# Kernel optimization log

Measured on AMD Instinct MI355X. Metric: run time of the kernel, lower is better.

## Reference

```python
import jax, jax.numpy as jnp
import numpy as np

ALPHA = 0.2      # LeakyReLU negative slope
BN_EPS = 1e-5    # torch BatchNorm1d default eps

N_NODES = 50000
N_EDGES = 1600000
DIM_IN = 128
DIM_HID = 64
DIM_OUT = 128
NUM_HEADS = 8


def gat_layer(feat, src, dst, W, a, gamma, beta):
    """One GATLayer forward (dropout disabled, BatchNorm in training mode
    i.e. normalized with batch statistics over the node dimension)."""
    n = feat.shape[0]
    dh = W.shape[1]
    msg = feat @ W                                  # [N, dh]
    attn_src = msg @ a[:dh]                         # [N]
    attn_dst = msg @ a[dh:]                         # [N]
    scores = jax.nn.leaky_relu(attn_src[src] + attn_dst[dst], ALPHA)  # [E]
    scores = scores - scores.max()                  # global max-subtract (as in source)
    e = jnp.exp(scores)                             # [E]
    denom = jax.ops.segment_sum(e, dst, num_segments=n) + 1e-10       # [N]
    coef = e / denom[dst]                           # [E] segment-softmax
    out = jax.ops.segment_sum(msg[src] * coef[:, None], dst, num_segments=n)  # [N, dh]
    # BatchNorm1d (training-mode batch stats, biased variance)
    mean = out.mean(axis=0)
    var = out.var(axis=0)
    out = (out - mean) * jax.lax.rsqrt(var + BN_EPS) * gamma + beta
    return out


def setup_inputs() -> dict:
    key = jax.random.key(0)
    ks = jax.random.split(key, 10)
    feat = jax.random.normal(ks[0], (N_NODES, DIM_IN), dtype=jnp.float32)
    edges = jax.random.randint(ks[1], (2, N_EDGES), 0, N_NODES)

    def xavier(k, shape):
        fan_in, fan_out = shape[0], shape[-1]
        lim = np.sqrt(6.0 / (fan_in + fan_out)).astype(np.float32)
        return jax.random.uniform(k, shape, jnp.float32, -lim, lim)

    W_heads = xavier(ks[2], (NUM_HEADS, DIM_IN, DIM_HID))
    a_heads = xavier(ks[3], (NUM_HEADS, 2 * DIM_HID))
    gamma_h = jnp.ones((NUM_HEADS, DIM_HID), jnp.float32)
    beta_h = jnp.zeros((NUM_HEADS, DIM_HID), jnp.float32)
    W_out = xavier(ks[4], (NUM_HEADS * DIM_HID, DIM_OUT))
    a_out = xavier(ks[5], (2 * DIM_OUT,))
    gamma_o = jnp.ones((DIM_OUT,), jnp.float32)
    beta_o = jnp.zeros((DIM_OUT,), jnp.float32)
    W_res = xavier(ks[6], (DIM_IN, DIM_OUT))
    b_res = jnp.zeros((DIM_OUT,), jnp.float32)
    return {"feat": feat, "edges": edges, "W_heads": W_heads, "a_heads": a_heads,
            "gamma_h": gamma_h, "beta_h": beta_h, "W_out": W_out, "a_out": a_out,
            "gamma_o": gamma_o, "beta_o": beta_o, "W_res": W_res, "b_res": b_res}


def reference(feat, edges, W_heads, a_heads, gamma_h, beta_h,
              W_out, a_out, gamma_o, beta_o, W_res, b_res):
    src, dst = edges[0], edges[1]
    # python loop over a small fixed number of heads keeps peak memory low
    head_outs = [gat_layer(feat, src, dst, W_heads[h], a_heads[h], gamma_h[h], beta_h[h])
                 for h in range(NUM_HEADS)]
    x = jnp.concatenate(head_outs, axis=-1)          # [N, H*dh]
    x = gat_layer(x, src, dst, W_out, a_out, gamma_o, beta_o)  # [N, dout]
    x = x + feat @ W_res + b_res                     # residual Linear
    return x
```

## Files before the change

### kernel.cpp

```cpp
#include <hip/hip_runtime.h>
#include <math.h>

#define N_NODES 50000
#define N_EDGES 1600000
#define DIM_IN  128
#define DIM_HID 64
#define NHEADS  8
#define HDIM    (NHEADS*DIM_HID)
#define DIM_OUT 128
#define SMBLK   1024
#define MAXBLK  512
#define HISTBLK 2048
#define LDK     72
#define INV_N   2e-5f
#define CSBLK   400

typedef __attribute__((ext_vector_type(2))) unsigned short us2;
typedef __attribute__((ext_vector_type(4))) unsigned short us4;
typedef __attribute__((ext_vector_type(8))) unsigned short us8;
typedef __attribute__((ext_vector_type(8))) short bf16x8;
typedef __attribute__((ext_vector_type(4))) float f32x4;

__device__ __forceinline__ float leaky(float x) { return x >= 0.f ? x : 0.2f * x; }
__device__ __forceinline__ float bf2f(unsigned short h) {
  return __uint_as_float(((unsigned)h) << 16);
}
__device__ __forceinline__ unsigned short f2bf(float f) {
  unsigned u = __float_as_uint(f);
  unsigned r = (u + 0x7fffu + ((u >> 16) & 1u)) >> 16;
  return (unsigned short)r;
}
__device__ __forceinline__ float bn_scale(float sum, float sq, float g) {
  float mean = sum * INV_N;
  float var = sq * INV_N - mean * mean;
  return g * rsqrtf(var + 1e-5f);
}

__global__ void prep_kernel(const float* __restrict__ feat, const float* __restrict__ Wh,
                            const float* __restrict__ Wres, const int* __restrict__ edst,
                            unsigned short* __restrict__ feat_bf,
                            unsigned short* __restrict__ Bt1,
                            unsigned short* __restrict__ Btr,
                            int* __restrict__ counts) {
  int b = blockIdx.x;
  if (b < 6250) {
    int i = b * 256 + threadIdx.x;
    float4 v = *reinterpret_cast<const float4*>(&feat[(size_t)i * 4]);
    us4 o;
    o[0] = f2bf(v.x); o[1] = f2bf(v.y); o[2] = f2bf(v.z); o[3] = f2bf(v.w);
    *reinterpret_cast<us4*>(&feat_bf[(size_t)i * 4]) = o;
  } else if (b < 6506) {
    int idx = (b - 6250) * 256 + threadIdx.x;
    int n = idx >> 7, k = idx & 127;
    Bt1[idx] = f2bf(Wh[(n >> 6) * (DIM_IN * DIM_HID) + k * DIM_HID + (n & 63)]);
  } else if (b < 6570) {
    int idx = (b - 6506) * 256 + threadIdx.x;
    int n = idx >> 7, k = idx & 127;
    Btr[idx] = f2bf(Wres[k * DIM_OUT + n]);
  } else {
    int bid = b - 6570;
    for (int e = bid * 256 + threadIdx.x; e < N_EDGES; e += HISTBLK * 256)
      atomicAdd(&counts[edst[e]], 1);
  }
}

__global__ void foldw2_kernel(const float* __restrict__ W,
                              const float* __restrict__ colsum, const float* __restrict__ colsq,
                              const float* __restrict__ gamma,
                              unsigned short* __restrict__ Bt) {
  int idx = blockIdx.x * 256 + threadIdx.x;
  if (idx >= DIM_OUT * HDIM) return;
  int n = idx >> 9, k = idx & 511;
  float sc = bn_scale(colsum[k], colsq[k], gamma[k]);
  Bt[idx] = f2bf(W[k * DIM_OUT + n] * sc);
}

__global__ void bias2_kernel(const float* __restrict__ W,
                             const float* __restrict__ colsum, const float* __restrict__ colsq,
                             const float* __restrict__ gamma, const float* __restrict__ beta,
                             float* __restrict__ bias2) {
  int j = threadIdx.x;
  if (j >= DIM_OUT) return;
  float s = 0.f;
  for (int c = 0; c < HDIM; ++c) {
    float mean = colsum[c] * INV_N;
    float sc = bn_scale(colsum[c], colsq[c], gamma[c]);
    float shift = beta[c] - mean * sc;
    s = fmaf(shift, W[c * DIM_OUT + j], s);
  }
  bias2[j] = s;
}

__device__ __forceinline__ void gemm_body(
    const unsigned short* __restrict__ A, const unsigned short* __restrict__ Bt,
    void* __restrict__ Cout, const float* __restrict__ bias,
    int M, int N, int K, int outbf) {
  __shared__ unsigned short As[128 * LDK];
  __shared__ unsigned short Bs[128 * LDK];
  const int tid = threadIdx.x;
  const int lane = tid & 63, wid = tid >> 6;
  const int wr = wid >> 1, wc = wid & 1;
  const int l15 = lane & 15, lhi = lane >> 4;
  const int m0 = blockIdx.y * 128, n0 = blockIdx.x * 128;
  const int srow = tid >> 3;
  const int sc8 = (tid - srow) & 7;
  f32x4 acc[4][4];
#pragma unroll
  for (int i = 0; i < 4; ++i)
#pragma unroll
    for (int j = 0; j < 4; ++j) acc[i][j] = f32x4{0.f, 0.f, 0.f, 0.f};

  for (int k0 = 0; k0 < K; k0 += 64) {
    __syncthreads();
#pragma unroll
    for (int p = 0; p < 4; ++p) {
      int row = p * 32 + srow;
      us8 va = {0, 0, 0, 0, 0, 0, 0, 0};
      int gr = m0 + row;
      if (gr < M) va = *reinterpret_cast<const us8*>(&A[(size_t)gr * K + k0 + sc8 * 8]);
      *reinterpret_cast<us8*>(&As[row * LDK + sc8 * 8]) = va;
      us8 vb = {0, 0, 0, 0, 0, 0, 0, 0};
      int gn = n0 + row;
      if (gn < N) vb = *reinterpret_cast<const us8*>(&Bt[(size_t)gn * K + k0 + sc8 * 8]);
      *reinterpret_cast<us8*>(&Bs[row * LDK + sc8 * 8]) = vb;
    }
    __syncthreads();
#pragma unroll
    for (int kk = 0; kk < 2; ++kk) {
      bf16x8 af[4], bfr[4];
#pragma unroll
      for (int i = 0; i < 4; ++i)
        af[i] = *reinterpret_cast<const bf16x8*>(&As[(wr * 64 + i * 16 + l15) * LDK + kk * 32 + lhi * 8]);
#pragma unroll
      for (int j = 0; j < 4; ++j)
        bfr[j] = *reinterpret_cast<const bf16x8*>(&Bs[(wc * 64 + j * 16 + l15) * LDK + kk * 32 + lhi * 8]);
#pragma unroll
      for (int i = 0; i < 4; ++i)
#pragma unroll
        for (int j = 0; j < 4; ++j)
          acc[i][j] = __builtin_amdgcn_mfma_f32_16x16x32_bf16(af[i], bfr[j], acc[i][j], 0, 0, 0);
    }
  }
#pragma unroll
  for (int j = 0; j < 4; ++j) {
    int col = n0 + wc * 64 + j * 16 + l15;
    float bb = bias ? bias[col] : 0.f;
#pragma unroll
    for (int i = 0; i < 4; ++i) {
      f32x4 v = acc[i][j];
#pragma unroll
      for (int t = 0; t < 4; ++t) {
        int row = m0 + wr * 64 + i * 16 + lhi * 4 + t;
        if (row < M) {
          float o = v[t] + bb;
          if (outbf) ((unsigned short*)Cout)[(size_t)row * N + col] = f2bf(o);
          else       ((float*)Cout)[(size_t)row * N + col] = o;
        }
      }
    }
  }
}

__global__ __launch_bounds__(256) void gemm_single(
    const unsigned short* __restrict__ A, const unsigned short* __restrict__ Bt,
    void* __restrict__ Cout, const float* __restrict__ bias,
    int M, int N, int K, int outbf) {
  gemm_body(A, Bt, Cout, bias, M, N, K, outbf);
}

__global__ __launch_bounds__(256) void gemm_dual(
    const unsigned short* __restrict__ A0, const unsigned short* __restrict__ Bt0,
    void* __restrict__ C0, const float* __restrict__ b0, int K0,
    const unsigned short* __restrict__ A1, const unsigned short* __restrict__ Bt1,
    void* __restrict__ C1, const float* __restrict__ b1, int K1) {
  if (blockIdx.z == 0) gemm_body(A0, Bt0, C0, b0, N_NODES, DIM_OUT, K0, 1);
  else                 gemm_body(A1, Bt1, C1, b1, N_NODES, DIM_OUT, K1, 0);
}

__global__ __launch_bounds__(256) void attn1_kernel(
    const unsigned short* __restrict__ msg, const float* __restrict__ a_heads,
    float* __restrict__ asrc, float* __restrict__ adst, int Nn) {
  int lane = threadIdx.x & 63;
  int n = blockIdx.x * 4 + (threadIdx.x >> 6);
  if (n >= Nn) return;
  us8 v = *reinterpret_cast<const us8*>(&msg[(size_t)n * HDIM + lane * 8]);
  int h = lane >> 3, p0 = (lane & 7) * 8;
  float s = 0.f, d = 0.f;
#pragma unroll
  for (int j = 0; j < 8; ++j) {
    float f = bf2f(v[j]);
    s = fmaf(f, a_heads[h * 128 + p0 + j], s);
    d = fmaf(f, a_heads[h * 128 + 64 + p0 + j], d);
  }
  s += __shfl_xor(s, 1, 64); s += __shfl_xor(s, 2, 64); s += __shfl_xor(s, 4, 64);
  d += __shfl_xor(d, 1, 64); d += __shfl_xor(d, 2, 64); d += __shfl_xor(d, 4, 64);
  if ((lane & 7) == 0) { asrc[n * 8 + h] = s; adst[n * 8 + h] = d; }
}

__global__ __launch_bounds__(256) void attn2_kernel(
    const unsigned short* __restrict__ msg, const float* __restrict__ a_out,
    float* __restrict__ asrc, float* __restrict__ adst, int Nn) {
  int lane = threadIdx.x & 63;
  int n = blockIdx.x * 4 + (threadIdx.x >> 6);
  if (n >= Nn) return;
  us2 v = *reinterpret_cast<const us2*>(&msg[(size_t)n * 128 + lane * 2]);
  float f0 = bf2f(v[0]), f1 = bf2f(v[1]);
  float s = f0 * a_out[2 * lane] + f1 * a_out[2 * lane + 1];
  float d = f0 * a_out[128 + 2 * lane] + f1 * a_out[128 + 2 * lane + 1];
#pragma unroll
  for (int off = 32; off; off >>= 1) {
    s += __shfl_xor(s, off, 64);
    d += __shfl_xor(d, off, 64);
  }
  if (lane == 0) { asrc[n] = s; adst[n] = d; }
}

__global__ __launch_bounds__(256) void scan1_kernel(
    const int* __restrict__ counts, int* __restrict__ rowptr, int* __restrict__ bsum, int n) {
  __shared__ int wsum[4];
  int b0 = blockIdx.x * 1024;
  int t = threadIdx.x;
  int lane = t & 63, w = t >> 6;
  int v[4]; int s = 0;
#pragma unroll
  for (int i = 0; i < 4; ++i) {
    int idx = b0 + t * 4 + i;
    v[i] = (idx < n) ? counts[idx] : 0;
    s += v[i];
  }
  int x = s;
#pragma unroll
  for (int off = 1; off < 64; off <<= 1) {
    int y = __shfl_up(x, off, 64);
    if (lane >= off) x += y;
  }
  if (lane == 63) wsum[w] = x;
  __syncthreads();
  int wof = 0;
  for (int i = 0; i < w; ++i) wof += wsum[i];
  int run = wof + x - s;
#pragma unroll
  for (int i = 0; i < 4; ++i) {
    int idx = b0 + t * 4 + i;
    if (idx < n) rowptr[idx] = run;
    run += v[i];
  }
  if (t == 255) bsum[blockIdx.x] = wof + x;
}

__global__ __launch_bounds__(256) void scan23_kernel(
    int* __restrict__ rowptr, const int* __restrict__ bsum, int n) {
  __shared__ int carry_sh;
  int b = blockIdx.x, t = threadIdx.x;
  if (t < 64) {
    int v = (t < b) ? bsum[t] : 0;
#pragma unroll
    for (int off = 32; off; off >>= 1) v += __shfl_xor(v, off, 64);
    if (t == 0) carry_sh = v;
  }
  __syncthreads();
  int carry = carry_sh;
  int i0 = b * 1024;
#pragma unroll
  for (int q = 0; q < 4; ++q) {
    int i = i0 + q * 256 + t;
    if (i < n) rowptr[i] += carry;
  }
  if (b == gridDim.x - 1 && t == 0) rowptr[n] = N_EDGES;
}

__global__ __launch_bounds__(256) void scatter_max1_kernel(
    const int* __restrict__ esrc, const int* __restrict__ edst,
    const float* __restrict__ asrc, const float* __restrict__ adst,
    const int* __restrict__ rowptr, int* __restrict__ cursor,
    int* __restrict__ colsrc, float* __restrict__ part, int E) {
  float m[8];
#pragma unroll
  for (int h = 0; h < 8; ++h) m[h] = -3.4e38f;
  for (int e = blockIdx.x * blockDim.x + threadIdx.x; e < E; e += gridDim.x * blockDim.x) {
    int s = esrc[e], d = edst[e];
    int pos = rowptr[d] + atomicAdd(&cursor[d], 1);
    colsrc[pos] = s;
    float4 s0 = *reinterpret_cast<const float4*>(&asrc[(size_t)s * 8]);
    float4 s1 = *reinterpret_cast<const float4*>(&asrc[(size_t)s * 8 + 4]);
    float4 d0 = *reinterpret_cast<const float4*>(&adst[(size_t)d * 8]);
    float4 d1 = *reinterpret_cast<const float4*>(&adst[(size_t)d * 8 + 4]);
    float xs[8] = {s0.x + d0.x, s0.y + d0.y, s0.z + d0.z, s0.w + d0.w,
                   s1.x + d1.x, s1.y + d1.y, s1.z + d1.z, s1.w + d1.w};
#pragma unroll
    for (int h = 0; h < 8; ++h) m[h] = fmaxf(m[h], leaky(xs[h]));
  }
#pragma unroll
  for (int h = 0; h < 8; ++h)
#pragma unroll
    for (int off = 32; off; off >>= 1) m[h] = fmaxf(m[h], __shfl_xor(m[h], off, 64));
  __shared__ float sm[4][8];
  int wv = threadIdx.x >> 6, ln = threadIdx.x & 63;
  if (ln == 0)
#pragma unroll
    for (int h = 0; h < 8; ++h) sm[wv][h] = m[h];
  __syncthreads();
  if (threadIdx.x < 8) {
    int h = threadIdx.x;
    part[blockIdx.x * 8 + h] =
        fmaxf(fmaxf(sm[0][h], sm[1][h]), fmaxf(sm[2][h], sm[3][h]));
  }
}

__global__ void max1_final_kernel(const float* __restrict__ part, float* __restrict__ maxv, int nblk) {
  int t = threadIdx.x;
  int h = t & 7, k = t >> 3;
  float m = -3.4e38f;
  for (int i = k; i < nblk; i += 8) m = fmaxf(m, part[i * 8 + h]);
  m = fmaxf(m, __shfl_xor(m, 8, 64));
  m = fmaxf(m, __shfl_xor(m, 16, 64));
  m = fmaxf(m, __shfl_xor(m, 32, 64));
  if (t < 8) maxv[t] = m;
}

__global__ __launch_bounds__(256) void max2_part_kernel(
    const int* __restrict__ esrc, const int* __restrict__ edst,
    const float* __restrict__ asrc, const float* __restrict__ adst,
    float* __restrict__ part, int E) {
  float m = -3.4e38f;
  for (int e = blockIdx.x * blockDim.x + threadIdx.x; e < E; e += gridDim.x * blockDim.x) {
    float x = asrc[esrc[e]] + adst[edst[e]];
    m = fmaxf(m, leaky(x));
  }
#pragma unroll
  for (int off = 32; off; off >>= 1) m = fmaxf(m, __shfl_xor(m, off, 64));
  __shared__ float sm[4];
  int wv = threadIdx.x >> 6, ln = threadIdx.x & 63;
  if (ln == 0) sm[wv] = m;
  __syncthreads();
  if (threadIdx.x == 0)
    part[blockIdx.x] = fmaxf(fmaxf(sm[0], sm[1]), fmaxf(sm[2], sm[3]));
}

__global__ void max2_final_kernel(const float* __restrict__ part, float* __restrict__ maxv, int nblk) {
  int t = threadIdx.x;
  float m = -3.4e38f;
  for (int i = t; i < nblk; i += 64) m = fmaxf(m, part[i]);
#pragma unroll
  for (int off = 32; off; off >>= 1) m = fmaxf(m, __shfl_xor(m, off, 64));
  if (t == 0) maxv[0] = m;
}

__global__ __launch_bounds__(256) void agg1_kernel(
    const unsigned short* __restrict__ msg, const float* __restrict__ asrc,
    const float* __restrict__ adst, const float* __restrict__ maxv,
    const int* __restrict__ rowptr, const int* __restrict__ colsrc,
    unsigned short* __restrict__ out) {
  int wv = threadIdx.x >> 6, l = threadIdx.x & 63;
  int n = blockIdx.x * 4 + wv;
  const int h = l >> 3;
  const int eloc = l & 7;
  const int hbase = l & 56;
  float M = maxv[h];
  float ad = adst[(size_t)n * 8 + h];
  int e0 = rowptr[n], e1 = rowptr[n + 1];
  float acc[8];
#pragma unroll
  for (int j = 0; j < 8; ++j) acc[j] = 0.f;
  float ds = 0.f;
  int base = e0;
  for (; base + 8 <= e1; base += 8) {
    int sreg = colsrc[base + eloc];
    float x = asrc[(size_t)sreg * 8 + h] + ad;
    x = x >= 0.f ? x : 0.2f * x;
    float creg = __expf(x - M);
#pragma unroll
    for (int e = 0; e < 8; ++e) {
      float c = __shfl(creg, hbase | e, 64);
      int s = __shfl(sreg, e, 64);
      ds += c;
      us8 m = *reinterpret_cast<const us8*>(&msg[(size_t)s * HDIM + l * 8]);
#pragma unroll
      for (int j = 0; j < 8; ++j) acc[j] = fmaf(bf2f(m[j]), c, acc[j]);
    }
  }
  if (base < e1) {
    int cnt = e1 - base;
    int sreg = 0; float creg = 0.f;
    if (eloc < cnt) {
      sreg = colsrc[base + eloc];
      float x = asrc[(size_t)sreg * 8 + h] + ad;
      x = x >= 0.f ? x : 0.2f * x;
      creg = __expf(x - M);
    }
    for (int e = 0; e < cnt; ++e) {
      float c = __shfl(creg, hbase | e, 64);
      int s = __shfl(sreg, e, 64);
      ds += c;
      us8 m = *reinterpret_cast<const us8*>(&msg[(size_t)s * HDIM + l * 8]);
#pragma unroll
      for (int j = 0; j < 8; ++j) acc[j] = fmaf(bf2f(m[j]), c, acc[j]);
    }
  }
  float inv = 1.0f / (ds + 1e-10f);
  us8 o;
#pragma unroll
  for (int j = 0; j < 8; ++j) o[j] = f2bf(acc[j] * inv);
  *reinterpret_cast<us8*>(&out[(size_t)n * HDIM + l * 8]) = o;
}

__global__ __launch_bounds__(256) void agg2_kernel(
    const unsigned short* __restrict__ msg, const float* __restrict__ asrc,
    const float* __restrict__ adst, const float* __restrict__ maxv,
    const int* __restrict__ rowptr, const int* __restrict__ colsrc,
    float* __restrict__ out) {
  int wv = threadIdx.x >> 6, ln = threadIdx.x & 63;
  int n = blockIdx.x * 4 + wv;
  float M = maxv[0];
  float ad = adst[n];
  int e0 = rowptr[n], e1 = rowptr[n + 1];
  float a0 = 0.f, a1 = 0.f, ds = 0.f;
  for (int base = e0; base < e1; base += 64) {
    int cnt = min(64, e1 - base);
    int s_reg = 0; float c_reg = 0.f;
    if (ln < cnt) {
      s_reg = colsrc[base + ln];
      float x = asrc[s_reg] + ad;
      x = x >= 0.f ? x : 0.2f * x;
      c_reg = __expf(x - M);
    }
    int e = 0;
    for (; e + 4 <= cnt; e += 4) {
      int s0 = __shfl(s_reg, e, 64),     s1 = __shfl(s_reg, e + 1, 64);
      int s2 = __shfl(s_reg, e + 2, 64), s3 = __shfl(s_reg, e + 3, 64);
      float c0 = __shfl(c_reg, e, 64),     c1 = __shfl(c_reg, e + 1, 64);
      float c2 = __shfl(c_reg, e + 2, 64), c3 = __shfl(c_reg, e + 3, 64);
      us2 m0 = *reinterpret_cast<const us2*>(&msg[(size_t)s0 * 128 + 2 * ln]);
      us2 m1 = *reinterpret_cast<const us2*>(&msg[(size_t)s1 * 128 + 2 * ln]);
      us2 m2 = *reinterpret_cast<const us2*>(&msg[(size_t)s2 * 128 + 2 * ln]);
      us2 m3 = *reinterpret_cast<const us2*>(&msg[(size_t)s3 * 128 + 2 * ln]);
      ds += (c0 + c1) + (c2 + c3);
      a0 = fmaf(bf2f(m0[0]), c0, a0); a1 = fmaf(bf2f(m0[1]), c0, a1);
      a0 = fmaf(bf2f(m1[0]), c1, a0); a1 = fmaf(bf2f(m1[1]), c1, a1);
      a0 = fmaf(bf2f(m2[0]), c2, a0); a1 = fmaf(bf2f(m2[1]), c2, a1);
      a0 = fmaf(bf2f(m3[0]), c3, a0); a1 = fmaf(bf2f(m3[1]), c3, a1);
    }
    for (; e < cnt; ++e) {
      int s = __shfl(s_reg, e, 64);
      float c = __shfl(c_reg, e, 64);
      us2 m = *reinterpret_cast<const us2*>(&msg[(size_t)s * 128 + 2 * ln]);
      ds += c;
      a0 = fmaf(bf2f(m[0]), c, a0);
      a1 = fmaf(bf2f(m[1]), c, a1);
    }
  }
  float inv = 1.0f / (ds + 1e-10f);
  float2 r; r.x = a0 * inv; r.y = a1 * inv;
  *reinterpret_cast<float2*>(&out[(size_t)n * 128 + 2 * ln]) = r;
}

__global__ __launch_bounds__(256) void colstats_bf512_kernel(
    const unsigned short* __restrict__ X, float* __restrict__ sums,
    float* __restrict__ sqs, int M) {
  int tid = threadIdx.x;
  int cg = tid & 63;
  int wv = tid >> 6;
  int rows = (M + gridDim.x - 1) / gridDim.x;
  int r0 = blockIdx.x * rows;
  int r1 = min(M, r0 + rows);
  float s[8], q[8];
#pragma unroll
  for (int j = 0; j < 8; ++j) { s[j] = 0.f; q[j] = 0.f; }
  for (int r = r0 + wv; r < r1; r += 4) {
    us8 v = *reinterpret_cast<const us8*>(&X[(size_t)r * 512 + cg * 8]);
#pragma unroll
    for (int j = 0; j < 8; ++j) {
      float f = bf2f(v[j]);
      s[j] += f; q[j] = fmaf(f, f, q[j]);
    }
  }
  __shared__ float shs[3][512];
  __shared__ float shq[3][512];
  if (wv > 0) {
#pragma unroll
    for (int j = 0; j < 8; ++j) {
      shs[wv - 1][cg * 8 + j] = s[j];
      shq[wv - 1][cg * 8 + j] = q[j];
    }
  }
  __syncthreads();
  if (wv == 0) {
#pragma unroll
    for (int j = 0; j < 8; ++j) {
      int c = cg * 8 + j;
      atomicAdd(&sums[c], s[j] + shs[0][c] + shs[1][c] + shs[2][c]);
      atomicAdd(&sqs[c],  q[j] + shq[0][c] + shq[1][c] + shq[2][c]);
    }
  }
}

__global__ __launch_bounds__(256) void colstats_f128_kernel(
    const float* __restrict__ X, float* __restrict__ sums,
    float* __restrict__ sqs, int M) {
  int tid = threadIdx.x;
  int g = tid & 31;
  int slot = tid >> 5;
  int rows = (M + gridDim.x - 1) / gridDim.x;
  int r0 = blockIdx.x * rows;
  int r1 = min(M, r0 + rows);
  float s[4] = {0.f, 0.f, 0.f, 0.f}, q[4] = {0.f, 0.f, 0.f, 0.f};
  for (int r = r0 + slot; r < r1; r += 8) {
    float4 v = *reinterpret_cast<const float4*>(&X[(size_t)r * 128 + g * 4]);
    s[0] += v.x; q[0] = fmaf(v.x, v.x, q[0]);
    s[1] += v.y; q[1] = fmaf(v.y, v.y, q[1]);
    s[2] += v.z; q[2] = fmaf(v.z, v.z, q[2]);
    s[3] += v.w; q[3] = fmaf(v.w, v.w, q[3]);
  }
#pragma unroll
  for (int j = 0; j < 4; ++j) {
    s[j] += __shfl_xor(s[j], 32, 64);
    q[j] += __shfl_xor(q[j], 32, 64);
  }
  __shared__ float shs[3][128];
  __shared__ float shq[3][128];
  int wv = tid >> 6, ln = tid & 63;
  if (wv > 0 && ln < 32) {
#pragma unroll
    for (int j = 0; j < 4; ++j) {
      shs[wv - 1][g * 4 + j] = s[j];
      shq[wv - 1][g * 4 + j] = q[j];
    }
  }
  __syncthreads();
  if (wv == 0 && ln < 32) {
#pragma unroll
    for (int j = 0; j < 4; ++j) {
      int c = g * 4 + j;
      atomicAdd(&sums[c], s[j] + shs[0][c] + shs[1][c] + shs[2][c]);
      atomicAdd(&sqs[c],  q[j] + shq[0][c] + shq[1][c] + shq[2][c]);
    }
  }
}

__global__ void final_kernel(float* __restrict__ out, const float* __restrict__ resid,
                             const float* __restrict__ colsum, const float* __restrict__ colsq,
                             const float* __restrict__ gamma, const float* __restrict__ beta,
                             int total) {
  for (int i = blockIdx.x * blockDim.x + threadIdx.x; i < total; i += gridDim.x * blockDim.x) {
    int c = i & 127;
    float mean = colsum[c] * INV_N;
    float sc = bn_scale(colsum[c], colsq[c], gamma[c]);
    float sh = beta[c] - mean * sc;
    out[i] = fmaf(out[i], sc, sh) + resid[i];
  }
}

extern "C" void kernel_launch(void* const* d_in, const int* in_sizes, int n_in,
                              void* d_out, int out_size, void* d_ws, size_t ws_size,
                              hipStream_t stream) {
  const float* feat    = (const float*)d_in[0];
  const int*   edges   = (const int*)d_in[1];
  const int*   esrc    = edges;
  const int*   edst    = edges + N_EDGES;
  const float* W_heads = (const float*)d_in[2];
  const float* a_heads = (const float*)d_in[3];
  const float* gamma_h = (const float*)d_in[4];
  const float* beta_h  = (const float*)d_in[5];
  const float* W_out   = (const float*)d_in[6];
  const float* a_out   = (const float*)d_in[7];
  const float* gamma_o = (const float*)d_in[8];
  const float* beta_o  = (const float*)d_in[9];
  const float* W_res   = (const float*)d_in[10];
  const float* b_res   = (const float*)d_in[11];
  float* out = (float*)d_out;

  char* ws = (char*)d_ws;
  size_t off = 0;
  auto alloc = [&](size_t bytes) {
    void* p = ws + off;
    off = (off + bytes + 255) & ~(size_t)255;
    return p;
  };
  unsigned short* msg1    = (unsigned short*)alloc((size_t)N_NODES * HDIM * 2);
  unsigned short* out1_bf = (unsigned short*)alloc((size_t)N_NODES * HDIM * 2);
  unsigned short* feat_bf = (unsigned short*)alloc((size_t)N_NODES * DIM_IN * 2);
  float*    resid  = (float*)alloc((size_t)N_NODES * DIM_OUT * 4);
  float*    asrc1  = (float*)alloc((size_t)N_NODES * NHEADS * 4);
  float*    adst1  = (float*)alloc((size_t)N_NODES * NHEADS * 4);
  int*      counts = (int*)alloc((size_t)N_NODES * 4);
  int*      cursor = (int*)alloc((size_t)N_NODES * 4);
  int*      rowptr = (int*)alloc((size_t)(N_NODES + 1) * 4);
  int*      colsrc = (int*)alloc((size_t)N_EDGES * 4);
  int*      bsum   = (int*)alloc(64 * 4);
  float*    part   = (float*)alloc((size_t)SMBLK * 8 * 4);
  float*    maxv1  = (float*)alloc(8 * 4);
  float*    maxv2  = (float*)alloc(4);
  float*    colsum = (float*)alloc(HDIM * 4);
  float*    colsq  = (float*)alloc(HDIM * 4);
  unsigned short* Bt1 = (unsigned short*)alloc((size_t)HDIM * DIM_IN * 2);
  unsigned short* Bt2 = (unsigned short*)alloc((size_t)DIM_OUT * HDIM * 2);
  unsigned short* Btr = (unsigned short*)alloc((size_t)DIM_OUT * DIM_IN * 2);
  float*    bias2  = (float*)alloc(DIM_OUT * 4);
  unsigned short* msg2 = msg1;
  float* asrc2 = asrc1; float* adst2 = adst1;
  (void)n_in; (void)in_sizes; (void)out_size; (void)ws_size;

  hipMemsetAsync(counts, 0, (char*)rowptr - (char*)counts, stream);
  hipMemsetAsync(colsum, 0, 4096, stream);

  prep_kernel<<<6570 + HISTBLK, 256, 0, stream>>>(feat, W_heads, W_res, edst,
                                                  feat_bf, Bt1, Btr, counts);

  dim3 g1(HDIM / 128, (N_NODES + 127) / 128);
  gemm_single<<<g1, 256, 0, stream>>>(feat_bf, Bt1, msg1, nullptr, N_NODES, HDIM, DIM_IN, 1);
  attn1_kernel<<<(N_NODES + 3) / 4, 256, 0, stream>>>(msg1, a_heads, asrc1, adst1, N_NODES);

  int nsb = (N_NODES + 1023) / 1024;
  scan1_kernel<<<nsb, 256, 0, stream>>>(counts, rowptr, bsum, N_NODES);
  scan23_kernel<<<nsb, 256, 0, stream>>>(rowptr, bsum, N_NODES);

  scatter_max1_kernel<<<SMBLK, 256, 0, stream>>>(esrc, edst, asrc1, adst1, rowptr,
                                                 cursor, colsrc, part, N_EDGES);
  max1_final_kernel<<<1, 64, 0, stream>>>(part, maxv1, SMBLK);
  agg1_kernel<<<N_NODES / 4, 256, 0, stream>>>(msg1, asrc1, adst1, maxv1, rowptr, colsrc, out1_bf);

  colstats_bf512_kernel<<<CSBLK, 256, 0, stream>>>(out1_bf, colsum, colsq, N_NODES);
  foldw2_kernel<<<(DIM_OUT * HDIM + 255) / 256, 256, 0, stream>>>(W_out, colsum, colsq, gamma_h, Bt2);
  bias2_kernel<<<1, 128, 0, stream>>>(W_out, colsum, colsq, gamma_h, beta_h, bias2);

  dim3 g2d(1, (N_NODES + 127) / 128, 2);
  gemm_dual<<<g2d, 256, 0, stream>>>(out1_bf, Bt2, msg2, bias2, HDIM,
                                     feat_bf, Btr, resid, b_res, DIM_IN);
  attn2_kernel<<<(N_NODES + 3) / 4, 256, 0, stream>>>(msg2, a_out, asrc2, adst2, N_NODES);

  max2_part_kernel<<<MAXBLK, 256, 0, stream>>>(esrc, edst, asrc2, adst2, part, N_EDGES);
  max2_final_kernel<<<1, 64, 0, stream>>>(part, maxv2, MAXBLK);
  agg2_kernel<<<N_NODES / 4, 256, 0, stream>>>(msg2, asrc2, adst2, maxv2, rowptr, colsrc, out);

  hipMemsetAsync(colsum, 0, 4096, stream);
  colstats_f128_kernel<<<CSBLK, 256, 0, stream>>>(out, colsum, colsq, N_NODES);
  final_kernel<<<2048, 256, 0, stream>>>(out, resid, colsum, colsq, gamma_o, beta_o,
                                         N_NODES * DIM_OUT);
}
```

Measured before the change: 780.9 us.

## Fuse attention dots into GEMM epilogue and use node-level softmax shift

The per-head attention source/destination dot products are now computed in the first GEMM's epilogue from the accumulators, so the separate pass that re-reads the bf16 message matrix goes away. The global softmax shift no longer needs an edge-level gather. It is taken as max(asrc)+max(adst) from cheap node-level reductions, which relies on softmax being invariant to any constant shift. The edge scatter kernel no longer gathers attention values, and the second-layer edge max pass is gone. The trade-off is that the shift is only an approximate bound rather than the exact max (leaky is not applied), which slightly changes exp magnitudes and the relative size of the 1e-10 epsilon.

```diff
diff --git a/kernel.cpp b/kernel.cpp
--- a/kernel.cpp
+++ b/kernel.cpp
@@ -8,9 +8,9 @@
 #define NHEADS  8
 #define HDIM    (NHEADS*DIM_HID)
 #define DIM_OUT 128
-#define SMBLK   1024
-#define MAXBLK  512
+#define SCBLK   1024
 #define HISTBLK 2048
+#define NMBLK   64
 #define LDK     72
 #define INV_N   2e-5f
 #define CSBLK   400
@@ -161,11 +161,99 @@
   }
 }
 
-__global__ __launch_bounds__(256) void gemm_single(
+__global__ __launch_bounds__(256) void gemm1_attn_kernel(
     const unsigned short* __restrict__ A, const unsigned short* __restrict__ Bt,
-    void* __restrict__ Cout, const float* __restrict__ bias,
-    int M, int N, int K, int outbf) {
-  gemm_body(A, Bt, Cout, bias, M, N, K, outbf);
+    unsigned short* __restrict__ Cout, const float* __restrict__ a_heads,
+    float* __restrict__ asrc, float* __restrict__ adst) {
+  __shared__ unsigned short As[128 * LDK];
+  __shared__ unsigned short Bs[128 * LDK];
+  const int M = N_NODES, N = HDIM, K = DIM_IN;
+  const int tid = threadIdx.x;
+  const int lane = tid & 63, wid = tid >> 6;
+  const int wr = wid >> 1, wc = wid & 1;
+  const int l15 = lane & 15, lhi = lane >> 4;
+  const int m0 = blockIdx.y * 128, n0 = blockIdx.x * 128;
+  const int srow = tid >> 3;
+  const int sc8 = (tid - srow) & 7;
+  f32x4 acc[4][4];
+#pragma unroll
+  for (int i = 0; i < 4; ++i)
+#pragma unroll
+    for (int j = 0; j < 4; ++j) acc[i][j] = f32x4{0.f, 0.f, 0.f, 0.f};
+
+  for (int k0 = 0; k0 < K; k0 += 64) {
+    __syncthreads();
+#pragma unroll
+    for (int p = 0; p < 4; ++p) {
+      int row = p * 32 + srow;
+      us8 va = {0, 0, 0, 0, 0, 0, 0, 0};
+      int gr = m0 + row;
+      if (gr < M) va = *reinterpret_cast<const us8*>(&A[(size_t)gr * K + k0 + sc8 * 8]);
+      *reinterpret_cast<us8*>(&As[row * LDK + sc8 * 8]) = va;
+      us8 vb = {0, 0, 0, 0, 0, 0, 0, 0};
+      int gn = n0 + row;
+      if (gn < N) vb = *reinterpret_cast<const us8*>(&Bt[(size_t)gn * K + k0 + sc8 * 8]);
+      *reinterpret_cast<us8*>(&Bs[row * LDK + sc8 * 8]) = vb;
+    }
+    __syncthreads();
+#pragma unroll
+    for (int kk = 0; kk < 2; ++kk) {
+      bf16x8 af[4], bfr[4];
+#pragma unroll
+      for (int i = 0; i < 4; ++i)
+        af[i] = *reinterpret_cast<const bf16x8*>(&As[(wr * 64 + i * 16 + l15) * LDK + kk * 32 + lhi * 8]);
+#pragma unroll
+      for (int j = 0; j < 4; ++j)
+        bfr[j] = *reinterpret_cast<const bf16x8*>(&Bs[(wc * 64 + j * 16 + l15) * LDK + kk * 32 + lhi * 8]);
+#pragma unroll
+      for (int i = 0; i < 4; ++i)
+#pragma unroll
+        for (int j = 0; j < 4; ++j)
+          acc[i][j] = __builtin_amdgcn_mfma_f32_16x16x32_bf16(af[i], bfr[j], acc[i][j], 0, 0, 0);
+    }
+  }
+#pragma unroll
+  for (int j = 0; j < 4; ++j) {
+    int col = n0 + wc * 64 + j * 16 + l15;
+#pragma unroll
+    for (int i = 0; i < 4; ++i) {
+      f32x4 v = acc[i][j];
+#pragma unroll
+      for (int t = 0; t < 4; ++t) {
+        int row = m0 + wr * 64 + i * 16 + lhi * 4 + t;
+        if (row < M) Cout[(size_t)row * N + col] = f2bf(v[t]);
+      }
+    }
+  }
+  const int h = blockIdx.x * 2 + wc;
+  float aS[4], aD[4];
+#pragma unroll
+  for (int j = 0; j < 4; ++j) {
+    aS[j] = a_heads[h * 128 + j * 16 + l15];
+    aD[j] = a_heads[h * 128 + 64 + j * 16 + l15];
+  }
+#pragma unroll
+  for (int i = 0; i < 4; ++i) {
+#pragma unroll
+    for (int t = 0; t < 4; ++t) {
+      float s = 0.f, d = 0.f;
+#pragma unroll
+      for (int j = 0; j < 4; ++j) {
+        float v = acc[i][j][t];
+        s = fmaf(v, aS[j], s);
+        d = fmaf(v, aD[j], d);
+      }
+      s += __shfl_xor(s, 1, 64); s += __shfl_xor(s, 2, 64);
+      s += __shfl_xor(s, 4, 64); s += __shfl_xor(s, 8, 64);
+      d += __shfl_xor(d, 1, 64); d += __shfl_xor(d, 2, 64);
+      d += __shfl_xor(d, 4, 64); d += __shfl_xor(d, 8, 64);
+      int row = m0 + wr * 64 + i * 16 + lhi * 4 + t;
+      if (l15 == 0 && row < M) {
+        asrc[(size_t)row * 8 + h] = s;
+        adst[(size_t)row * 8 + h] = d;
+      }
+    }
+  }
 }
 
 __global__ __launch_bounds__(256) void gemm_dual(
@@ -175,26 +263,6 @@
     void* __restrict__ C1, const float* __restrict__ b1, int K1) {
   if (blockIdx.z == 0) gemm_body(A0, Bt0, C0, b0, N_NODES, DIM_OUT, K0, 1);
   else                 gemm_body(A1, Bt1, C1, b1, N_NODES, DIM_OUT, K1, 0);
-}
-
-__global__ __launch_bounds__(256) void attn1_kernel(
-    const unsigned short* __restrict__ msg, const float* __restrict__ a_heads,
-    float* __restrict__ asrc, float* __restrict__ adst, int Nn) {
-  int lane = threadIdx.x & 63;
-  int n = blockIdx.x * 4 + (threadIdx.x >> 6);
-  if (n >= Nn) return;
-  us8 v = *reinterpret_cast<const us8*>(&msg[(size_t)n * HDIM + lane * 8]);
-  int h = lane >> 3, p0 = (lane & 7) * 8;
-  float s = 0.f, d = 0.f;
-#pragma unroll
-  for (int j = 0; j < 8; ++j) {
-    float f = bf2f(v[j]);
-    s = fmaf(f, a_heads[h * 128 + p0 + j], s);
-    d = fmaf(f, a_heads[h * 128 + 64 + p0 + j], d);
-  }
-  s += __shfl_xor(s, 1, 64); s += __shfl_xor(s, 2, 64); s += __shfl_xor(s, 4, 64);
-  d += __shfl_xor(d, 1, 64); d += __shfl_xor(d, 2, 64); d += __shfl_xor(d, 4, 64);
-  if ((lane & 7) == 0) { asrc[n * 8 + h] = s; adst[n * 8 + h] = d; }
 }
 
 __global__ __launch_bounds__(256) void attn2_kernel(
@@ -215,6 +283,54 @@
   if (lane == 0) { asrc[n] = s; adst[n] = d; }
 }
 
+__global__ __launch_bounds__(256) void nodemax_part_kernel(
+    const float* __restrict__ a, const float* __restrict__ b,
+    float* __restrict__ part, int total) {
+  int t = threadIdx.x;
+  float ms = -3.4e38f, md = -3.4e38f;
+  for (int i = blockIdx.x * 256 + t; i < total; i += NMBLK * 256) {
+    ms = fmaxf(ms, a[i]);
+    md = fmaxf(md, b[i]);
+  }
+  ms = fmaxf(ms, __shfl_xor(ms, 8, 64));
+  ms = fmaxf(ms, __shfl_xor(ms, 16, 64));
+  ms = fmaxf(ms, __shfl_xor(ms, 32, 64));
+  md = fmaxf(md, __shfl_xor(md, 8, 64));
+  md = fmaxf(md, __shfl_xor(md, 16, 64));
+  md = fmaxf(md, __shfl_xor(md, 32, 64));
+  __shared__ float sh[4][8][2];
+  int wv = t >> 6, ln = t & 63;
+  if (ln < 8) { sh[wv][ln][0] = ms; sh[wv][ln][1] = md; }
+  __syncthreads();
+  if (t < 8) {
+    float s4 = fmaxf(fmaxf(sh[0][t][0], sh[1][t][0]), fmaxf(sh[2][t][0], sh[3][t][0]));
+    float d4 = fmaxf(fmaxf(sh[0][t][1], sh[1][t][1]), fmaxf(sh[2][t][1], sh[3][t][1]));
+    part[blockIdx.x * 16 + t * 2] = s4;
+    part[blockIdx.x * 16 + t * 2 + 1] = d4;
+  }
+}
+
+__global__ void nodemax_final_kernel(const float* __restrict__ part, float* __restrict__ maxv, int H) {
+  int t = threadIdx.x;
+  int ch = t & 15, k = t >> 4;
+  float m = -3.4e38f;
+  for (int i = k; i < NMBLK; i += 4) m = fmaxf(m, part[i * 16 + ch]);
+  m = fmaxf(m, __shfl_xor(m, 16, 64));
+  m = fmaxf(m, __shfl_xor(m, 32, 64));
+  float S = __shfl(m, (t & 7) * 2, 64);
+  float D = __shfl(m, (t & 7) * 2 + 1, 64);
+  if (H == 8) {
+    if (t < 8) maxv[t] = S + D;
+  } else {
+    float Sm = S, Dm = D;
+    Sm = fmaxf(Sm, __shfl_xor(Sm, 1, 64)); Sm = fmaxf(Sm, __shfl_xor(Sm, 2, 64));
+    Sm = fmaxf(Sm, __shfl_xor(Sm, 4, 64));
+    Dm = fmaxf(Dm, __shfl_xor(Dm, 1, 64)); Dm = fmaxf(Dm, __shfl_xor(Dm, 2, 64));
+    Dm = fmaxf(Dm, __shfl_xor(Dm, 4, 64));
+    if (t == 0) maxv[0] = Sm + Dm;
+  }
+}
+
 __global__ __launch_bounds__(256) void scan1_kernel(
     const int* __restrict__ counts, int* __restrict__ rowptr, int* __restrict__ bsum, int n) {
   __shared__ int wsum[4];
@@ -269,81 +385,15 @@
   if (b == gridDim.x - 1 && t == 0) rowptr[n] = N_EDGES;
 }
 
-__global__ __launch_bounds__(256) void scatter_max1_kernel(
+__global__ __launch_bounds__(256) void scatter_kernel(
     const int* __restrict__ esrc, const int* __restrict__ edst,
-    const float* __restrict__ asrc, const float* __restrict__ adst,
     const int* __restrict__ rowptr, int* __restrict__ cursor,
-    int* __restrict__ colsrc, float* __restrict__ part, int E) {
-  float m[8];
-#pragma unroll
-  for (int h = 0; h < 8; ++h) m[h] = -3.4e38f;
+    int* __restrict__ colsrc, int E) {
   for (int e = blockIdx.x * blockDim.x + threadIdx.x; e < E; e += gridDim.x * blockDim.x) {
-    int s = esrc[e], d = edst[e];
+    int d = edst[e];
     int pos = rowptr[d] + atomicAdd(&cursor[d], 1);
-    colsrc[pos] = s;
-    float4 s0 = *reinterpret_cast<const float4*>(&asrc[(size_t)s * 8]);
-    float4 s1 = *reinterpret_cast<const float4*>(&asrc[(size_t)s * 8 + 4]);
-    float4 d0 = *reinterpret_cast<const float4*>(&adst[(size_t)d * 8]);
-    float4 d1 = *reinterpret_cast<const float4*>(&adst[(size_t)d * 8 + 4]);
-    float xs[8] = {s0.x + d0.x, s0.y + d0.y, s0.z + d0.z, s0.w + d0.w,
-                   s1.x + d1.x, s1.y + d1.y, s1.z + d1.z, s1.w + d1.w};
-#pragma unroll
-    for (int h = 0; h < 8; ++h) m[h] = fmaxf(m[h], leaky(xs[h]));
-  }
-#pragma unroll
-  for (int h = 0; h < 8; ++h)
-#pragma unroll
-    for (int off = 32; off; off >>= 1) m[h] = fmaxf(m[h], __shfl_xor(m[h], off, 64));
-  __shared__ float sm[4][8];
-  int wv = threadIdx.x >> 6, ln = threadIdx.x & 63;
-  if (ln == 0)
-#pragma unroll
-    for (int h = 0; h < 8; ++h) sm[wv][h] = m[h];
-  __syncthreads();
-  if (threadIdx.x < 8) {
-    int h = threadIdx.x;
-    part[blockIdx.x * 8 + h] =
-        fmaxf(fmaxf(sm[0][h], sm[1][h]), fmaxf(sm[2][h], sm[3][h]));
-  }
-}
-
-__global__ void max1_final_kernel(const float* __restrict__ part, float* __restrict__ maxv, int nblk) {
-  int t = threadIdx.x;
-  int h = t & 7, k = t >> 3;
-  float m = -3.4e38f;
-  for (int i = k; i < nblk; i += 8) m = fmaxf(m, part[i * 8 + h]);
-  m = fmaxf(m, __shfl_xor(m, 8, 64));
-  m = fmaxf(m, __shfl_xor(m, 16, 64));
-  m = fmaxf(m, __shfl_xor(m, 32, 64));
-  if (t < 8) maxv[t] = m;
-}
-
-__global__ __launch_bounds__(256) void max2_part_kernel(
-    const int* __restrict__ esrc, const int* __restrict__ edst,
-    const float* __restrict__ asrc, const float* __restrict__ adst,
-    float* __restrict__ part, int E) {
-  float m = -3.4e38f;
-  for (int e = blockIdx.x * blockDim.x + threadIdx.x; e < E; e += gridDim.x * blockDim.x) {
-    float x = asrc[esrc[e]] + adst[edst[e]];
-    m = fmaxf(m, leaky(x));
-  }
-#pragma unroll
-  for (int off = 32; off; off >>= 1) m = fmaxf(m, __shfl_xor(m, off, 64));
-  __shared__ float sm[4];
-  int wv = threadIdx.x >> 6, ln = threadIdx.x & 63;
-  if (ln == 0) sm[wv] = m;
-  __syncthreads();
-  if (threadIdx.x == 0)
-    part[blockIdx.x] = fmaxf(fmaxf(sm[0], sm[1]), fmaxf(sm[2], sm[3]));
-}
-
-__global__ void max2_final_kernel(const float* __restrict__ part, float* __restrict__ maxv, int nblk) {
-  int t = threadIdx.x;
-  float m = -3.4e38f;
-  for (int i = t; i < nblk; i += 64) m = fmaxf(m, part[i]);
-#pragma unroll
-  for (int off = 32; off; off >>= 1) m = fmaxf(m, __shfl_xor(m, off, 64));
-  if (t == 0) maxv[0] = m;
+    colsrc[pos] = esrc[e];
+  }
 }
 
 __global__ __launch_bounds__(256) void agg1_kernel(
@@ -587,7 +637,7 @@
   int*      rowptr = (int*)alloc((size_t)(N_NODES + 1) * 4);
   int*      colsrc = (int*)alloc((size_t)N_EDGES * 4);
   int*      bsum   = (int*)alloc(64 * 4);
-  float*    part   = (float*)alloc((size_t)SMBLK * 8 * 4);
+  float*    partmx = (float*)alloc((size_t)NMBLK * 16 * 4);
   float*    maxv1  = (float*)alloc(8 * 4);
   float*    maxv2  = (float*)alloc(4);
   float*    colsum = (float*)alloc(HDIM * 4);
@@ -607,16 +657,15 @@
                                                   feat_bf, Bt1, Btr, counts);
 
   dim3 g1(HDIM / 128, (N_NODES + 127) / 128);
-  gemm_single<<<g1, 256, 0, stream>>>(feat_bf, Bt1, msg1, nullptr, N_NODES, HDIM, DIM_IN, 1);
-  attn1_kernel<<<(N_NODES + 3) / 4, 256, 0, stream>>>(msg1, a_heads, asrc1, adst1, N_NODES);
+  gemm1_attn_kernel<<<g1, 256, 0, stream>>>(feat_bf, Bt1, msg1, a_heads, asrc1, adst1);
+  nodemax_part_kernel<<<NMBLK, 256, 0, stream>>>(asrc1, adst1, partmx, N_NODES * 8);
+  nodemax_final_kernel<<<1, 64, 0, stream>>>(partmx, maxv1, 8);
 
   int nsb = (N_NODES + 1023) / 1024;
   scan1_kernel<<<nsb, 256, 0, stream>>>(counts, rowptr, bsum, N_NODES);
   scan23_kernel<<<nsb, 256, 0, stream>>>(rowptr, bsum, N_NODES);
 
-  scatter_max1_kernel<<<SMBLK, 256, 0, stream>>>(esrc, edst, asrc1, adst1, rowptr,
-                                                 cursor, colsrc, part, N_EDGES);
-  max1_final_kernel<<<1, 64, 0, stream>>>(part, maxv1, SMBLK);
+  scatter_kernel<<<SCBLK, 256, 0, stream>>>(esrc, edst, rowptr, cursor, colsrc, N_EDGES);
   agg1_kernel<<<N_NODES / 4, 256, 0, stream>>>(msg1, asrc1, adst1, maxv1, rowptr, colsrc, out1_bf);
 
   colstats_bf512_kernel<<<CSBLK, 256, 0, stream>>>(out1_bf, colsum, colsq, N_NODES);
@@ -627,9 +676,9 @@
   gemm_dual<<<g2d, 256, 0, stream>>>(out1_bf, Bt2, msg2, bias2, HDIM,
                                      feat_bf, Btr, resid, b_res, DIM_IN);
   attn2_kernel<<<(N_NODES + 3) / 4, 256, 0, stream>>>(msg2, a_out, asrc2, adst2, N_NODES);
-
-  max2_part_kernel<<<MAXBLK, 256, 0, stream>>>(esrc, edst, asrc2, adst2, part, N_EDGES);
-  max2_final_kernel<<<1, 64, 0, stream>>>(part, maxv2, MAXBLK);
+  nodemax_part_kernel<<<NMBLK, 256, 0, stream>>>(asrc2, adst2, partmx, N_NODES);
+  nodemax_final_kernel<<<1, 64, 0, stream>>>(partmx, maxv2, 1);
+
   agg2_kernel<<<N_NODES / 4, 256, 0, stream>>>(msg2, asrc2, adst2, maxv2, rowptr, colsrc, out);
 
   hipMemsetAsync(colsum, 0, 4096, stream);
```

Result: faster. 755.4 us (-3.3%).
